# Optimization experiments

Measured on AMD Instinct MI355X. Metric: run time of the kernel, lower is better.

Reference implementation:

```python
import jax, jax.numpy as jnp
import numpy as np

B, S, D = 4, 2048, 1024
H = 16
DH = D // H


def setup_inputs() -> dict:
    key = jax.random.key(0)
    ks = jax.random.split(key, 9)
    s = 0.02
    return {
        "x": jax.random.normal(ks[0], (B, S, D), dtype=jnp.float32),
        "Wq": jax.random.normal(ks[1], (D, D), dtype=jnp.float32) * s,
        "bq": jax.random.normal(ks[2], (D,), dtype=jnp.float32) * s,
        "Wk": jax.random.normal(ks[3], (D, D), dtype=jnp.float32) * s,
        "bk": jax.random.normal(ks[4], (D,), dtype=jnp.float32) * s,
        "Wv": jax.random.normal(ks[5], (D, D), dtype=jnp.float32) * s,
        "bv": jax.random.normal(ks[6], (D,), dtype=jnp.float32) * s,
        "Wo": jax.random.normal(ks[7], (D, D), dtype=jnp.float32) * s,
        "bo": jax.random.normal(ks[8], (D,), dtype=jnp.float32) * s,
    }


def _split_heads(t):
    # [B,S,D] -> [B,H,S,DH]
    b, s, d = t.shape
    return t.reshape(b, s, H, DH).transpose(0, 2, 1, 3)


def reference(x, Wq, bq, Wk, bk, Wv, bv, Wo, bo):
    q = _split_heads(x @ Wq.T + bq)
    k = _split_heads(x @ Wk.T + bk)
    v = _split_heads(x @ Wv.T + bv)
    scale = 1.0 / np.sqrt(DH).astype(np.float32)
    scores = jnp.einsum("bhqd,bhkd->bhqk", q, k) * scale  # [B,H,S,S]
    s = scores.shape[-2]
    causal = jnp.tril(jnp.ones((s, s), dtype=bool))
    scores = jnp.where(causal[None, None], scores, -jnp.inf)
    probs = jax.nn.softmax(scores, axis=-1)
    out = jnp.einsum("bhqk,bhkd->bhqd", probs, v)  # [B,H,S,DH]
    out = out.transpose(0, 2, 1, 3).reshape(x.shape[0], s, D)
    return out @ Wo.T + bo
```

## Files before the change

### kernel.cpp

```cpp
#include <hip/hip_runtime.h>
#include <hip/hip_bf16.h>
#include <cstdint>
#include <cstddef>


typedef unsigned short u16;
typedef __bf16 bf16x8 __attribute__((ext_vector_type(8)));
typedef float  f32x4  __attribute__((ext_vector_type(4)));

__device__ __forceinline__ u16 f2bf(float f) {
  unsigned u = __float_as_uint(f);
  unsigned r = u + 0x7fffu + ((u >> 16) & 1u);
  return (u16)(r >> 16);
}

__device__ __forceinline__ void llds16(const u16* g, u16* l) {
  __builtin_amdgcn_global_load_lds(
      (const __attribute__((address_space(1))) void*)g,
      (__attribute__((address_space(3))) void*)l, 16, 0, 0);
}

__global__ void cast_bf16_kernel(const float* __restrict__ in, u16* __restrict__ out, int n4) {
  int i = blockIdx.x * blockDim.x + threadIdx.x;
  if (i >= n4) return;
  float4 f = ((const float4*)in)[i];
  ushort4 u;
  u.x = f2bf(f.x); u.y = f2bf(f.y); u.z = f2bf(f.z); u.w = f2bf(f.w);
  ((ushort4*)out)[i] = u;
}

__global__ void cast4_kernel(const float* __restrict__ a, const float* __restrict__ b,
                             const float* __restrict__ c, const float* __restrict__ d,
                             u16* __restrict__ oa, u16* __restrict__ ob,
                             u16* __restrict__ oc, u16* __restrict__ od, int n4) {
  const int w = blockIdx.y;
  const float* src = (w == 0) ? a : (w == 1) ? b : (w == 2) ? c : d;
  u16* dst = (w == 0) ? oa : (w == 1) ? ob : (w == 2) ? oc : od;
  int i = blockIdx.x * blockDim.x + threadIdx.x;
  if (i >= n4) return;
  float4 f = ((const float4*)src)[i];
  ushort4 u;
  u.x = f2bf(f.x); u.y = f2bf(f.y); u.z = f2bf(f.z); u.w = f2bf(f.w);
  ((ushort4*)dst)[i] = u;
}

__global__ __launch_bounds__(512) void gemm_qkv_256(
    const u16* __restrict__ A, const u16* __restrict__ Bw,
    const float* __restrict__ b0, const float* __restrict__ b1, const float* __restrict__ b2,
    u16* __restrict__ qkv_out)
{
  __shared__ u16 lds[57344];

  const int tid = threadIdx.x;
  const int lane = tid & 63;
  const int wave = tid >> 6;

  const int bid = (int)blockIdx.x;
  const int xcd = bid & 7;
  const int idx = bid >> 3;
  const int mt = (xcd << 2) | (idx & 3);
  const int nt = idx >> 2;
  const int m0 = mt << 8;
  const int n0 = nt * 192;

  const int warp_m = wave >> 2;
  const int warp_n = wave & 3;
  const int wm = warp_m << 7;
  const int wn = warp_n * 48;
  const int fr = lane & 15;
  const int g  = lane >> 4;

  const int srow = tid >> 3;
  const int schk = ((tid & 7) ^ (srow & 7)) << 3;
  const u16* pA = A  + (size_t)(m0 + srow) * 1024 + schk;
  const u16* pB = Bw + (size_t)(n0 + srow) * 1024 + schk;

  const int rsw0 = ((g    ) ^ (fr & 7)) << 3;
  const int rsw1 = ((g ^ 4) ^ (fr & 7)) << 3;

  const u16* Ab0 = lds + (size_t)(wm + fr) * 64;
  const u16* Bb0 = lds + 16384 + (size_t)(wn + fr) * 64;
  const u16* Ab1 = Ab0 + 28672;
  const u16* Bb1 = Bb0 + 28672;

  f32x4 acc[8][3];
  const f32x4 zero = {0.f, 0.f, 0.f, 0.f};
#pragma unroll
  for (int i = 0; i < 8; i++)
#pragma unroll
    for (int j = 0; j < 3; j++) acc[i][j] = zero;

  bf16x8 a_[4][2];
  bf16x8 b_[3][2];

  auto stageA = [&](int kt, int buf, int half) {
    const u16* src = pA + (size_t)half * 131072 + (kt << 6);
    u16* dst = lds + buf * 28672 + half * 8192 + tid * 8;
    llds16(src, dst);
    llds16(src + 65536, dst + 4096);
  };
  auto stageB0 = [&](int kt, int buf) {
    const u16* src = pB + (kt << 6);
    u16* dst = lds + buf * 28672 + 16384 + tid * 8;
    llds16(src, dst);
    llds16(src + 65536, dst + 4096);
  };
  auto stageB1 = [&](int kt, int buf) {
    const u16* src = pB + 131072 + (kt << 6);
    u16* dst = lds + buf * 28672 + 24576 + tid * 8;
    llds16(src, dst);
  };
  auto loadA4 = [&](const u16* Ab, int ib) {
#pragma unroll
    for (int ii = 0; ii < 4; ii++) {
      const u16* r = Ab + (ib + ii) * 1024;
      a_[ii][0] = *(const bf16x8*)(r + rsw0);
      a_[ii][1] = *(const bf16x8*)(r + rsw1);
    }
  };
  auto loadB = [&](const u16* Bb, int j0, int nj) {
#pragma unroll
    for (int jj = 0; jj < 3; jj++) {
      if (jj < nj) {
        const u16* r = Bb + (j0 + jj) * 1024;
        b_[j0 + jj][0] = *(const bf16x8*)(r + rsw0);
        b_[j0 + jj][1] = *(const bf16x8*)(r + rsw1);
      }
    }
  };
  auto mfmaQ = [&](int ib, int j0, int nj) {
    __builtin_amdgcn_s_setprio(1);
#pragma unroll
    for (int jj = 0; jj < 3; jj++) {
      if (jj < nj) {
#pragma unroll
        for (int ii = 0; ii < 4; ii++) {
          acc[ib+ii][j0+jj] = __builtin_amdgcn_mfma_f32_16x16x32_bf16(
              a_[ii][0], b_[j0+jj][0], acc[ib+ii][j0+jj], 0, 0, 0);
          acc[ib+ii][j0+jj] = __builtin_amdgcn_mfma_f32_16x16x32_bf16(
              a_[ii][1], b_[j0+jj][1], acc[ib+ii][j0+jj], 0, 0, 0);
        }
      }
    }
    __builtin_amdgcn_s_setprio(0);
  };

  stageA(0, 0, 0);
  stageA(0, 0, 1);
  stageB0(0, 0);
  stageB1(0, 0);
  stageA(1, 1, 0);
  asm volatile("s_waitcnt vmcnt(2)" ::: "memory");
  __builtin_amdgcn_s_barrier();

  const int NTI = 8;
  for (int t = 0; t < NTI; ++t) {
    const bool st = (t < NTI - 1);
    const int ka = 2 * t + 1;
    const int kb = 2 * t + 2;
    const int kc = 2 * t + 3;

    loadA4(Ab0, 0); loadB(Bb0, 0, 2);
    stageA(ka, 1, 1);
    __builtin_amdgcn_s_barrier();
    mfmaQ(0, 0, 2);
    __builtin_amdgcn_s_barrier();
    loadB(Bb0, 2, 1);
    stageB0(ka, 1);
    __builtin_amdgcn_s_barrier();
    mfmaQ(0, 2, 1);
    __builtin_amdgcn_s_barrier();
    loadA4(Ab0, 4);
    stageB1(ka, 1);
    __builtin_amdgcn_s_barrier();
    mfmaQ(4, 2, 1);
    __builtin_amdgcn_s_barrier();
    if (st) stageA(kb, 0, 0);
    __builtin_amdgcn_s_barrier();
    mfmaQ(4, 0, 2);
    if (st) { asm volatile("s_waitcnt vmcnt(2)" ::: "memory"); }
    else    { asm volatile("s_waitcnt vmcnt(0)" ::: "memory"); }
    __builtin_amdgcn_s_barrier();

    loadA4(Ab1, 0); loadB(Bb1, 0, 2);
    if (st) stageA(kb, 0, 1);
    __builtin_amdgcn_s_barrier();
    mfmaQ(0, 0, 2);
    __builtin_amdgcn_s_barrier();
    loadB(Bb1, 2, 1);
    if (st) stageB0(kb, 0);
    __builtin_amdgcn_s_barrier();
    mfmaQ(0, 2, 1);
    __builtin_amdgcn_s_barrier();
    loadA4(Ab1, 4);
    if (st) stageB1(kb, 0);
    __builtin_amdgcn_s_barrier();
    mfmaQ(4, 2, 1);
    __builtin_amdgcn_s_barrier();
    if (st) stageA(kc, 1, 0);
    __builtin_amdgcn_s_barrier();
    mfmaQ(4, 0, 2);
    if (st) { asm volatile("s_waitcnt vmcnt(2)" ::: "memory"); }
    __builtin_amdgcn_s_barrier();
  }

  __syncthreads();
  const int bI  = m0 >> 11;
  const int s0m = m0 & 2047;
#pragma unroll
  for (int j = 0; j < 3; j++) {
    const int ncol = n0 + wn + j * 16 + fr;
    const int which = ncol >> 10;
    const float bb = ((which == 0) ? b0 : (which == 1) ? b1 : b2)[ncol & 1023];
    const float post = (which == 0) ? 0.18033688011f : 1.0f;
    const int cl = wn + j * 16 + fr;
#pragma unroll
    for (int i = 0; i < 8; i++) {
#pragma unroll
      for (int r = 0; r < 4; r++) {
        const int row = wm + i * 16 + g * 4 + r;
        lds[row * 200 + cl] = f2bf((acc[i][j][r] + bb) * post);
      }
    }
  }
  __syncthreads();
  const int part = tid & 7;
#pragma unroll
  for (int p = 0; p < 12; p++) {
    const int hc = p >> 2;
    const int ml = ((p & 3) << 6) + (tid >> 3);
    const int ncol0 = n0 + hc * 64;
    const int which = ncol0 >> 10;
    const int h = (ncol0 >> 6) & 15;
    const bf16x8 v = *(const bf16x8*)(lds + ml * 200 + hc * 64 + part * 8);
    *(bf16x8*)(qkv_out + (size_t)which * 8388608 +
               ((size_t)(bI * 16 + h) * 2048 + s0m + ml) * 64 + part * 8) = v;
  }
}

__global__ __launch_bounds__(256) void gemm_bt(
    const u16* __restrict__ A, const u16* __restrict__ Bw,
    const float* __restrict__ b0, const float* __restrict__ b1, const float* __restrict__ b2,
    u16* __restrict__ qkv_out, float* __restrict__ flat_out,
    int K, int mode)
{
  __shared__ u16 As[128 * 32];
  __shared__ u16 Bs[128 * 32];

  const int tid = threadIdx.x;
  const int n0 = blockIdx.x * 128;
  const int m0 = blockIdx.y * 128;

  const int srow = tid >> 2;
  const int soff = (tid & 3) * 8;
  const u16* gA0 = A  + (size_t)(m0 + srow) * K + soff;
  const u16* gA1 = gA0 + (size_t)64 * K;
  const u16* gB0 = Bw + (size_t)(n0 + srow) * K + soff;
  const u16* gB1 = gB0 + (size_t)64 * K;
  u16* lA0 = As + tid * 8;
  u16* lA1 = As + 2048 + tid * 8;
  u16* lB0 = Bs + tid * 8;
  u16* lB1 = Bs + 2048 + tid * 8;

  const int lane = tid & 63;
  const int wave = tid >> 6;
  const int wm = (wave >> 1) * 64;
  const int wn = (wave & 1) * 64;
  const int fr = lane & 15;
  const int k8 = (lane >> 4) * 8;

  f32x4 zero = {0.f, 0.f, 0.f, 0.f};
  f32x4 acc[4][4];
#pragma unroll
  for (int i = 0; i < 4; i++)
#pragma unroll
    for (int j = 0; j < 4; j++) acc[i][j] = zero;

  for (int k0 = 0; k0 < K; k0 += 32) {
    llds16(gA0 + k0, lA0);
    llds16(gA1 + k0, lA1);
    llds16(gB0 + k0, lB0);
    llds16(gB1 + k0, lB1);
    __syncthreads();
    bf16x8 af[4], bfr[4];
#pragma unroll
    for (int i = 0; i < 4; i++)
      af[i] = *(const bf16x8*)(As + (wm + i * 16 + fr) * 32 + k8);
#pragma unroll
    for (int j = 0; j < 4; j++)
      bfr[j] = *(const bf16x8*)(Bs + (wn + j * 16 + fr) * 32 + k8);
#pragma unroll
    for (int i = 0; i < 4; i++)
#pragma unroll
      for (int j = 0; j < 4; j++)
        acc[i][j] = __builtin_amdgcn_mfma_f32_16x16x32_bf16(af[i], bfr[j], acc[i][j], 0, 0, 0);
    __syncthreads();
  }

  const int rbase = (lane >> 4) * 4;
  if (mode == 0) {
    const int which = n0 >> 10;
    const float* bias = (which == 0) ? b0 : ((which == 1) ? b1 : b2);
    const float post = (which == 0) ? 0.18033688011f : 1.0f;
    u16* outb = qkv_out + (size_t)which * 8388608;
#pragma unroll
    for (int j = 0; j < 4; j++) {
      const int nn = (n0 + wn + j * 16 + fr) & 1023;
      const float bb = bias[nn];
      const int h = nn >> 6, dh = nn & 63;
#pragma unroll
      for (int i = 0; i < 4; i++) {
#pragma unroll
        for (int r = 0; r < 4; r++) {
          const int m = m0 + wm + i * 16 + rbase + r;
          const int bI = m >> 11, s = m & 2047;
          outb[(((size_t)bI * 16 + h) * 2048 + s) * 64 + dh] = f2bf((acc[i][j][r] + bb) * post);
        }
      }
    }
  } else {
#pragma unroll
    for (int j = 0; j < 4; j++) {
      const int n = n0 + wn + j * 16 + fr;
      const float bb = b0[n];
#pragma unroll
      for (int i = 0; i < 4; i++) {
#pragma unroll
        for (int r = 0; r < 4; r++) {
          const int m = m0 + wm + i * 16 + rbase + r;
          flat_out[(size_t)m * 1024 + n] = acc[i][j][r] + bb;
        }
      }
    }
  }
}

__global__ __launch_bounds__(256) void transpose_v(const u16* __restrict__ V, u16* __restrict__ VT) {
  __shared__ u16 t_s[64 * 72];
  const int tid = threadIdx.x;
  const int st = blockIdx.x << 6;
  const int bh = blockIdx.y;
  const u16* src = V + ((size_t)bh * 2048 + st) * 64;
#pragma unroll
  for (int p = 0; p < 2; p++) {
    int i = p * 256 + tid;
    int row = i >> 3, ch = i & 7;
    bf16x8 v = *(const bf16x8*)(src + row * 64 + ch * 8);
    *(bf16x8*)(t_s + row * 72 + ch * 8) = v;
  }
  __syncthreads();
  u16* dst = VT + (size_t)bh * 131072 + st;
#pragma unroll
  for (int p = 0; p < 2; p++) {
    int i = p * 256 + tid;
    int dh = i >> 3, ch = i & 7;
    union { u16 s[8]; bf16x8 v; } u;
#pragma unroll
    for (int e = 0; e < 8; e++) u.s[e] = t_s[(ch * 8 + e) * 72 + dh];
    *(bf16x8*)(dst + (size_t)dh * 2048 + ch * 8) = u.v;
  }
}

__global__ __launch_bounds__(256, 3) void attn_fa(
    const u16* __restrict__ Qb, const u16* __restrict__ Kb,
    const u16* __restrict__ VT, u16* __restrict__ Ob)
{
  __shared__ u16 k_s[2 * 4096];
  __shared__ u16 v_s[2 * 4096];
  __shared__ u16 p_s[128 * 72];
  __shared__ float l_s[128];

  const int tid = threadIdx.x;
  const int lane = tid & 63;
  const int wave = tid >> 6;
  const int bid = (int)blockIdx.x;
  const int qt = 15 - (bid >> 6);
  const int bh = (((bid >> 3) & 7) << 3) | (bid & 7);
  const size_t head = (size_t)bh << 17;
  const int fr = lane & 15;
  const int g = lane >> 4;
  const int k8 = g << 3;
  const int q0 = qt << 7;
  const int wrow = wave << 5;

  bf16x8 aq[2][2];
#pragma unroll
  for (int f = 0; f < 2; f++) {
    const u16* qp = Qb + head + (size_t)(q0 + wrow + (f << 4) + fr) * 64;
    aq[f][0] = *(const bf16x8*)(qp + k8);
    aq[f][1] = *(const bf16x8*)(qp + 32 + k8);
  }

  const int r0 = tid >> 3, c0 = tid & 7;
  const int r1 = 32 + r0;
  const int koff0 = r0 * 64 + (((c0 ^ r0) & 7) << 3);
  const int koff1 = r1 * 64 + (((c0 ^ r1) & 7) << 3);
  const int voff0 = r0 * 2048 + (((c0 ^ r0) & 7) << 3);
  const int voff1 = r1 * 2048 + (((c0 ^ r1) & 7) << 3);
  int kaddr[4][2], vaddr[2][4];
#pragma unroll
  for (int j = 0; j < 4; j++) {
    const int kn = (j << 4) + fr;
    kaddr[j][0] = kn * 64 + (((g ^ kn) & 7) << 3);
    kaddr[j][1] = kn * 64 + ((((g + 4) ^ kn) & 7) << 3);
#pragma unroll
    for (int s2 = 0; s2 < 2; s2++)
      vaddr[s2][j] = kn * 64 + ((((s2 << 2) + g) ^ (kn & 7)) << 3);
  }
  u16* const prow0 = p_s + (wrow + fr) * 72;
  u16* const prow1 = p_s + (wrow + 16 + fr) * 72;
  const u16* Kbase = Kb + head;
  const u16* Vbase = VT + head;

  auto issueK = [&](int jt2, int buf) {
    const u16* Kt = Kbase + ((size_t)jt2 << 12);
    llds16(Kt + koff0, k_s + (buf << 12) + tid * 8);
    llds16(Kt + koff1, k_s + (buf << 12) + 2048 + tid * 8);
  };
  auto issueV = [&](int jt2, int buf) {
    const u16* Vt = Vbase + (jt2 << 6);
    llds16(Vt + voff0, v_s + (buf << 12) + tid * 8);
    llds16(Vt + voff1, v_s + (buf << 12) + 2048 + tid * 8);
  };

  f32x4 o_acc[2][4];
  const f32x4 zero = {0.f, 0.f, 0.f, 0.f};
#pragma unroll
  for (int f = 0; f < 2; f++)
#pragma unroll
    for (int j = 0; j < 4; j++) o_acc[f][j] = zero;
  float l_run[2] = {0.f, 0.f};

  const int jmax = 2 * qt + 1;
  const int jt_diag = 2 * qt + (wave >> 1);

  auto do_pv = [&](const u16* vs) {
#pragma unroll
    for (int s2 = 0; s2 < 2; s2++) {
      const bf16x8 ap0 = *(const bf16x8*)(prow0 + (s2 << 5) + k8);
      const bf16x8 ap1 = *(const bf16x8*)(prow1 + (s2 << 5) + k8);
#pragma unroll
      for (int j = 0; j < 4; j++) {
        const bf16x8 bv = *(const bf16x8*)(vs + vaddr[s2][j]);
        o_acc[0][j] = __builtin_amdgcn_mfma_f32_16x16x32_bf16(ap0, bv, o_acc[0][j], 0, 0, 0);
        o_acc[1][j] = __builtin_amdgcn_mfma_f32_16x16x32_bf16(ap1, bv, o_acc[1][j], 0, 0, 0);
      }
    }
  };

  auto do_s = [&](const u16* ks, bool dodiag, int jt) {
    f32x4 s_acc[2][4];
#pragma unroll
    for (int f = 0; f < 2; f++)
#pragma unroll
      for (int j = 0; j < 4; j++) s_acc[f][j] = zero;
#pragma unroll
    for (int j = 0; j < 4; j++) {
      const bf16x8 ka0 = *(const bf16x8*)(ks + kaddr[j][0]);
      const bf16x8 ka1 = *(const bf16x8*)(ks + kaddr[j][1]);
      s_acc[0][j] = __builtin_amdgcn_mfma_f32_16x16x32_bf16(ka0, aq[0][0], s_acc[0][j], 0, 0, 0);
      s_acc[0][j] = __builtin_amdgcn_mfma_f32_16x16x32_bf16(ka1, aq[0][1], s_acc[0][j], 0, 0, 0);
      s_acc[1][j] = __builtin_amdgcn_mfma_f32_16x16x32_bf16(ka0, aq[1][0], s_acc[1][j], 0, 0, 0);
      s_acc[1][j] = __builtin_amdgcn_mfma_f32_16x16x32_bf16(ka1, aq[1][1], s_acc[1][j], 0, 0, 0);
    }
#pragma unroll
    for (int f = 0; f < 2; f++) {
      const int qa = q0 + wrow + (f << 4) + fr;
      u16* prow = (f == 0) ? prow0 : prow1;
      if (dodiag) {
#pragma unroll
        for (int j = 0; j < 4; j++) {
          const int kb = (jt << 6) + (j << 4) + (g << 2);
          float p0 = (kb + 0 > qa) ? 0.f : __builtin_amdgcn_exp2f(s_acc[f][j][0]);
          float p1 = (kb + 1 > qa) ? 0.f : __builtin_amdgcn_exp2f(s_acc[f][j][1]);
          float p2 = (kb + 2 > qa) ? 0.f : __builtin_amdgcn_exp2f(s_acc[f][j][2]);
          float p3 = (kb + 3 > qa) ? 0.f : __builtin_amdgcn_exp2f(s_acc[f][j][3]);
          l_run[f] += (p0 + p1) + (p2 + p3);
          union { __hip_bfloat162 h; unsigned u; } ca, cb;
          ca.h = __float22bfloat162_rn(make_float2(p0, p1));
          cb.h = __float22bfloat162_rn(make_float2(p2, p3));
          *(uint2*)(prow + (j << 4) + (g << 2)) = make_uint2(ca.u, cb.u);
        }
      } else {
#pragma unroll
        for (int j = 0; j < 4; j++) {
          float p0 = __builtin_amdgcn_exp2f(s_acc[f][j][0]);
          float p1 = __builtin_amdgcn_exp2f(s_acc[f][j][1]);
          float p2 = __builtin_amdgcn_exp2f(s_acc[f][j][2]);
          float p3 = __builtin_amdgcn_exp2f(s_acc[f][j][3]);
          l_run[f] += (p0 + p1) + (p2 + p3);
          union { __hip_bfloat162 h; unsigned u; } ca, cb;
          ca.h = __float22bfloat162_rn(make_float2(p0, p1));
          cb.h = __float22bfloat162_rn(make_float2(p2, p3));
          *(uint2*)(prow + (j << 4) + (g << 2)) = make_uint2(ca.u, cb.u);
        }
      }
    }
  };

  issueK(0, 0);

  for (int jt = 0; jt <= jmax; jt++) {
    const int kb = jt & 1;
    __syncthreads();
    if (jt < jmax) issueK(jt + 1, kb ^ 1);
    issueV(jt, kb);
    if (jt > 0 && jt - 1 <= jt_diag) do_pv(v_s + ((kb ^ 1) << 12));
    if (jt <= jt_diag) do_s(k_s + (kb << 12), jt == jt_diag, jt);
  }
  __syncthreads();
  if (jt_diag == jmax) do_pv(v_s + ((jmax & 1) << 12));

#pragma unroll
  for (int f = 0; f < 2; f++) {
    float l = l_run[f];
    l += __shfl_xor(l, 16);
    l += __shfl_xor(l, 32);
    if (g == 0) l_s[wrow + (f << 4) + fr] = l;
  }
  const int b = bh >> 4, h = bh & 15;
#pragma unroll
  for (int f = 0; f < 2; f++) {
#pragma unroll
    for (int r = 0; r < 4; r++) {
      const int qloc = wrow + (f << 4) + (g << 2) + r;
      const float inv = 1.f / l_s[qloc];
      const int q_abs = q0 + qloc;
#pragma unroll
      for (int j = 0; j < 4; j++)
        Ob[((size_t)b * 2048 + q_abs) * 1024 + (h << 6) + (j << 4) + fr] =
            f2bf(o_acc[f][j][r] * inv);
    }
  }
}

extern "C" void kernel_launch(void* const* d_in, const int* in_sizes, int n_in,
                              void* d_out, int out_size, void* d_ws, size_t ws_size,
                              hipStream_t stream) {
  const float* x  = (const float*)d_in[0];
  const float* Wq = (const float*)d_in[1];
  const float* bq = (const float*)d_in[2];
  const float* Wk = (const float*)d_in[3];
  const float* bk = (const float*)d_in[4];
  const float* Wv = (const float*)d_in[5];
  const float* bv = (const float*)d_in[6];
  const float* Wo = (const float*)d_in[7];
  const float* bo = (const float*)d_in[8];
  float* out = (float*)d_out;

  char* ws = (char*)d_ws;
  u16* xb    = (u16*)(ws);
  u16* vT    = (u16*)(ws);
  u16* wqkv  = (u16*)(ws + 16777216);
  u16* wo    = (u16*)(ws + 23068672);
  u16* qkv   = (u16*)(ws + 25165824);
  u16* attnb = (u16*)(ws + 75497472);

  cast_bf16_kernel<<<8192, 256, 0, stream>>>(x, xb, 2097152);
  cast4_kernel<<<dim3(1024, 4), 256, 0, stream>>>(
      Wq, Wk, Wv, Wo, wqkv, wqkv + 1048576, wqkv + 2097152, wo, 262144);

  gemm_qkv_256<<<dim3(512), 512, 0, stream>>>(xb, wqkv, bq, bk, bv, qkv);

  transpose_v<<<dim3(32, 64), 256, 0, stream>>>(qkv + 16777216, vT);

  attn_fa<<<dim3(1024), 256, 0, stream>>>(qkv, qkv + 8388608, vT, attnb);

  gemm_bt<<<dim3(8, 64), 256, 0, stream>>>(attnb, wo, bo, bo, bo, nullptr, out, 1024, 1);
}
```

Before: 247.7 us.

## Replace output projection GEMM with pipelined 256x128 tile kernel and reorder QKV MFMA phases

The simple 128x128 output-projection GEMM, which loaded one K=32 slice per step with full syncs, is replaced by a 512-thread 256x128-tile kernel. The new kernel uses swizzled LDS double buffering, direct global-to-LDS loads interleaved with MFMA phases, and an XCD-aware block mapping. The QKV GEMM's MFMA schedule is also reordered so all 8 A fragments stay in registers and the third B column is done in one pass. This costs more registers in exchange for fewer LDS reloads. The aim is to raise MFMA utilisation and cut synchronisation and memory stalls in both GEMMs.

After: 242.0 us. 1.02x faster.

```diff
diff --git a/kernel.cpp b/kernel.cpp
--- a/kernel.cpp
+++ b/kernel.cpp
@@ -90,7 +90,7 @@
 #pragma unroll
     for (int j = 0; j < 3; j++) acc[i][j] = zero;
 
-  bf16x8 a_[4][2];
+  bf16x8 a_[8][2];
   bf16x8 b_[3][2];
 
   auto stageA = [&](int kt, int buf, int half) {
@@ -114,8 +114,8 @@
 #pragma unroll
     for (int ii = 0; ii < 4; ii++) {
       const u16* r = Ab + (ib + ii) * 1024;
-      a_[ii][0] = *(const bf16x8*)(r + rsw0);
-      a_[ii][1] = *(const bf16x8*)(r + rsw1);
+      a_[ib + ii][0] = *(const bf16x8*)(r + rsw0);
+      a_[ib + ii][1] = *(const bf16x8*)(r + rsw1);
     }
   };
   auto loadB = [&](const u16* Bb, int j0, int nj) {
@@ -128,19 +128,27 @@
       }
     }
   };
-  auto mfmaQ = [&](int ib, int j0, int nj) {
+  auto mfmaJ01 = [&](int ib) {
     __builtin_amdgcn_s_setprio(1);
 #pragma unroll
-    for (int jj = 0; jj < 3; jj++) {
-      if (jj < nj) {
-#pragma unroll
-        for (int ii = 0; ii < 4; ii++) {
-          acc[ib+ii][j0+jj] = __builtin_amdgcn_mfma_f32_16x16x32_bf16(
-              a_[ii][0], b_[j0+jj][0], acc[ib+ii][j0+jj], 0, 0, 0);
-          acc[ib+ii][j0+jj] = __builtin_amdgcn_mfma_f32_16x16x32_bf16(
-              a_[ii][1], b_[j0+jj][1], acc[ib+ii][j0+jj], 0, 0, 0);
-        }
+    for (int jj = 0; jj < 2; jj++)
+#pragma unroll
+      for (int ii = 0; ii < 4; ii++) {
+        acc[ib+ii][jj] = __builtin_amdgcn_mfma_f32_16x16x32_bf16(
+            a_[ib+ii][0], b_[jj][0], acc[ib+ii][jj], 0, 0, 0);
+        acc[ib+ii][jj] = __builtin_amdgcn_mfma_f32_16x16x32_bf16(
+            a_[ib+ii][1], b_[jj][1], acc[ib+ii][jj], 0, 0, 0);
       }
+    __builtin_amdgcn_s_setprio(0);
+  };
+  auto mfmaJ2 = [&]() {
+    __builtin_amdgcn_s_setprio(1);
+#pragma unroll
+    for (int ii = 0; ii < 8; ii++) {
+      acc[ii][2] = __builtin_amdgcn_mfma_f32_16x16x32_bf16(
+          a_[ii][0], b_[2][0], acc[ii][2], 0, 0, 0);
+      acc[ii][2] = __builtin_amdgcn_mfma_f32_16x16x32_bf16(
+          a_[ii][1], b_[2][1], acc[ii][2], 0, 0, 0);
     }
     __builtin_amdgcn_s_setprio(0);
   };
@@ -163,21 +171,18 @@
     loadA4(Ab0, 0); loadB(Bb0, 0, 2);
     stageA(ka, 1, 1);
     __builtin_amdgcn_s_barrier();
-    mfmaQ(0, 0, 2);
+    mfmaJ01(0);
+    __builtin_amdgcn_s_barrier();
+    loadA4(Ab0, 4);
+    stageB0(ka, 1);
+    __builtin_amdgcn_s_barrier();
+    mfmaJ01(4);
     __builtin_amdgcn_s_barrier();
     loadB(Bb0, 2, 1);
-    stageB0(ka, 1);
-    __builtin_amdgcn_s_barrier();
-    mfmaQ(0, 2, 1);
-    __builtin_amdgcn_s_barrier();
-    loadA4(Ab0, 4);
     stageB1(ka, 1);
-    __builtin_amdgcn_s_barrier();
-    mfmaQ(4, 2, 1);
-    __builtin_amdgcn_s_barrier();
     if (st) stageA(kb, 0, 0);
     __builtin_amdgcn_s_barrier();
-    mfmaQ(4, 0, 2);
+    mfmaJ2();
     if (st) { asm volatile("s_waitcnt vmcnt(2)" ::: "memory"); }
     else    { asm volatile("s_waitcnt vmcnt(0)" ::: "memory"); }
     __builtin_amdgcn_s_barrier();
@@ -185,21 +190,17 @@
     loadA4(Ab1, 0); loadB(Bb1, 0, 2);
     if (st) stageA(kb, 0, 1);
     __builtin_amdgcn_s_barrier();
-    mfmaQ(0, 0, 2);
+    mfmaJ01(0);
+    __builtin_amdgcn_s_barrier();
+    loadA4(Ab1, 4);
+    if (st) stageB0(kb, 0);
+    __builtin_amdgcn_s_barrier();
+    mfmaJ01(4);
     __builtin_amdgcn_s_barrier();
     loadB(Bb1, 2, 1);
-    if (st) stageB0(kb, 0);
-    __builtin_amdgcn_s_barrier();
-    mfmaQ(0, 2, 1);
-    __builtin_amdgcn_s_barrier();
-    loadA4(Ab1, 4);
-    if (st) stageB1(kb, 0);
-    __builtin_amdgcn_s_barrier();
-    mfmaQ(4, 2, 1);
-    __builtin_amdgcn_s_barrier();
-    if (st) stageA(kc, 1, 0);
-    __builtin_amdgcn_s_barrier();
-    mfmaQ(4, 0, 2);
+    if (st) { stageB1(kb, 0); stageA(kc, 1, 0); }
+    __builtin_amdgcn_s_barrier();
+    mfmaJ2();
     if (st) { asm volatile("s_waitcnt vmcnt(2)" ::: "memory"); }
     __builtin_amdgcn_s_barrier();
   }
@@ -238,98 +239,165 @@
   }
 }
 
-__global__ __launch_bounds__(256) void gemm_bt(
+__global__ __launch_bounds__(512) void gemm_o_256(
     const u16* __restrict__ A, const u16* __restrict__ Bw,
-    const float* __restrict__ b0, const float* __restrict__ b1, const float* __restrict__ b2,
-    u16* __restrict__ qkv_out, float* __restrict__ flat_out,
-    int K, int mode)
+    const float* __restrict__ bo, float* __restrict__ out)
 {
-  __shared__ u16 As[128 * 32];
-  __shared__ u16 Bs[128 * 32];
+  __shared__ u16 lds[49152];
 
   const int tid = threadIdx.x;
-  const int n0 = blockIdx.x * 128;
-  const int m0 = blockIdx.y * 128;
-
-  const int srow = tid >> 2;
-  const int soff = (tid & 3) * 8;
-  const u16* gA0 = A  + (size_t)(m0 + srow) * K + soff;
-  const u16* gA1 = gA0 + (size_t)64 * K;
-  const u16* gB0 = Bw + (size_t)(n0 + srow) * K + soff;
-  const u16* gB1 = gB0 + (size_t)64 * K;
-  u16* lA0 = As + tid * 8;
-  u16* lA1 = As + 2048 + tid * 8;
-  u16* lB0 = Bs + tid * 8;
-  u16* lB1 = Bs + 2048 + tid * 8;
-
   const int lane = tid & 63;
   const int wave = tid >> 6;
-  const int wm = (wave >> 1) * 64;
-  const int wn = (wave & 1) * 64;
+
+  const int bid = (int)blockIdx.x;
+  const int xcd = bid & 7;
+  const int idx = bid >> 3;
+  const int mt = (xcd << 2) | (idx & 3);
+  const int nt = idx >> 2;
+  const int m0 = mt << 8;
+  const int n0 = nt << 7;
+
+  const int warp_m = wave >> 2;
+  const int warp_n = wave & 3;
+  const int wm = warp_m << 7;
+  const int wn = warp_n << 5;
   const int fr = lane & 15;
-  const int k8 = (lane >> 4) * 8;
-
-  f32x4 zero = {0.f, 0.f, 0.f, 0.f};
-  f32x4 acc[4][4];
-#pragma unroll
-  for (int i = 0; i < 4; i++)
-#pragma unroll
-    for (int j = 0; j < 4; j++) acc[i][j] = zero;
-
-  for (int k0 = 0; k0 < K; k0 += 32) {
-    llds16(gA0 + k0, lA0);
-    llds16(gA1 + k0, lA1);
-    llds16(gB0 + k0, lB0);
-    llds16(gB1 + k0, lB1);
-    __syncthreads();
-    bf16x8 af[4], bfr[4];
-#pragma unroll
-    for (int i = 0; i < 4; i++)
-      af[i] = *(const bf16x8*)(As + (wm + i * 16 + fr) * 32 + k8);
-#pragma unroll
-    for (int j = 0; j < 4; j++)
-      bfr[j] = *(const bf16x8*)(Bs + (wn + j * 16 + fr) * 32 + k8);
-#pragma unroll
-    for (int i = 0; i < 4; i++)
-#pragma unroll
-      for (int j = 0; j < 4; j++)
-        acc[i][j] = __builtin_amdgcn_mfma_f32_16x16x32_bf16(af[i], bfr[j], acc[i][j], 0, 0, 0);
-    __syncthreads();
-  }
-
-  const int rbase = (lane >> 4) * 4;
-  if (mode == 0) {
-    const int which = n0 >> 10;
-    const float* bias = (which == 0) ? b0 : ((which == 1) ? b1 : b2);
-    const float post = (which == 0) ? 0.18033688011f : 1.0f;
-    u16* outb = qkv_out + (size_t)which * 8388608;
-#pragma unroll
-    for (int j = 0; j < 4; j++) {
-      const int nn = (n0 + wn + j * 16 + fr) & 1023;
-      const float bb = bias[nn];
-      const int h = nn >> 6, dh = nn & 63;
-#pragma unroll
-      for (int i = 0; i < 4; i++) {
-#pragma unroll
-        for (int r = 0; r < 4; r++) {
-          const int m = m0 + wm + i * 16 + rbase + r;
-          const int bI = m >> 11, s = m & 2047;
-          outb[(((size_t)bI * 16 + h) * 2048 + s) * 64 + dh] = f2bf((acc[i][j][r] + bb) * post);
-        }
+  const int g  = lane >> 4;
+
+  const int srow = tid >> 3;
+  const int schk = ((tid & 7) ^ (srow & 7)) << 3;
+  const u16* pA = A  + (size_t)(m0 + srow) * 1024 + schk;
+  const u16* pB = Bw + (size_t)(n0 + srow) * 1024 + schk;
+
+  const int rsw0 = ((g    ) ^ (fr & 7)) << 3;
+  const int rsw1 = ((g ^ 4) ^ (fr & 7)) << 3;
+
+  const u16* Ab0 = lds + (size_t)(wm + fr) * 64;
+  const u16* Bb0 = lds + 16384 + (size_t)(wn + fr) * 64;
+  const u16* Ab1 = Ab0 + 24576;
+  const u16* Bb1 = Bb0 + 24576;
+
+  f32x4 acc[8][2];
+  const f32x4 zero = {0.f, 0.f, 0.f, 0.f};
+#pragma unroll
+  for (int i = 0; i < 8; i++)
+#pragma unroll
+    for (int j = 0; j < 2; j++) acc[i][j] = zero;
+
+  bf16x8 a_[8][2];
+  bf16x8 b_[2][2];
+
+  auto stageA = [&](int kt, int buf, int half) {
+    const u16* src = pA + (size_t)half * 131072 + (kt << 6);
+    u16* dst = lds + buf * 24576 + half * 8192 + tid * 8;
+    llds16(src, dst);
+    llds16(src + 65536, dst + 4096);
+  };
+  auto stageB = [&](int kt, int buf) {
+    const u16* src = pB + (kt << 6);
+    u16* dst = lds + buf * 24576 + 16384 + tid * 8;
+    llds16(src, dst);
+    llds16(src + 65536, dst + 4096);
+  };
+  auto loadA4 = [&](const u16* Ab, int ib) {
+#pragma unroll
+    for (int ii = 0; ii < 4; ii++) {
+      const u16* r = Ab + (ib + ii) * 1024;
+      a_[ib + ii][0] = *(const bf16x8*)(r + rsw0);
+      a_[ib + ii][1] = *(const bf16x8*)(r + rsw1);
+    }
+  };
+  auto loadB2 = [&](const u16* Bb) {
+#pragma unroll
+    for (int jj = 0; jj < 2; jj++) {
+      const u16* r = Bb + jj * 1024;
+      b_[jj][0] = *(const bf16x8*)(r + rsw0);
+      b_[jj][1] = *(const bf16x8*)(r + rsw1);
+    }
+  };
+  auto mfma16 = [&](int ib) {
+    __builtin_amdgcn_s_setprio(1);
+#pragma unroll
+    for (int jj = 0; jj < 2; jj++)
+#pragma unroll
+      for (int ii = 0; ii < 4; ii++) {
+        acc[ib+ii][jj] = __builtin_amdgcn_mfma_f32_16x16x32_bf16(
+            a_[ib+ii][0], b_[jj][0], acc[ib+ii][jj], 0, 0, 0);
+        acc[ib+ii][jj] = __builtin_amdgcn_mfma_f32_16x16x32_bf16(
+            a_[ib+ii][1], b_[jj][1], acc[ib+ii][jj], 0, 0, 0);
       }
-    }
-  } else {
-#pragma unroll
-    for (int j = 0; j < 4; j++) {
-      const int n = n0 + wn + j * 16 + fr;
-      const float bb = b0[n];
-#pragma unroll
-      for (int i = 0; i < 4; i++) {
-#pragma unroll
-        for (int r = 0; r < 4; r++) {
-          const int m = m0 + wm + i * 16 + rbase + r;
-          flat_out[(size_t)m * 1024 + n] = acc[i][j][r] + bb;
-        }
+    __builtin_amdgcn_s_setprio(0);
+  };
+  auto mfma8 = [&](int ib, int jj) {
+    __builtin_amdgcn_s_setprio(1);
+#pragma unroll
+    for (int ii = 0; ii < 4; ii++) {
+      acc[ib+ii][jj] = __builtin_amdgcn_mfma_f32_16x16x32_bf16(
+          a_[ib+ii][0], b_[jj][0], acc[ib+ii][jj], 0, 0, 0);
+      acc[ib+ii][jj] = __builtin_amdgcn_mfma_f32_16x16x32_bf16(
+          a_[ib+ii][1], b_[jj][1], acc[ib+ii][jj], 0, 0, 0);
+    }
+    __builtin_amdgcn_s_setprio(0);
+  };
+
+  stageA(0, 0, 0);
+  stageA(0, 0, 1);
+  stageB(0, 0);
+  stageA(1, 1, 0);
+  asm volatile("s_waitcnt vmcnt(2)" ::: "memory");
+  __builtin_amdgcn_s_barrier();
+
+  const int NTI = 8;
+  for (int t = 0; t < NTI; ++t) {
+    const bool st = (t < NTI - 1);
+    const int ka = 2 * t + 1;
+    const int kb = 2 * t + 2;
+    const int kc = 2 * t + 3;
+
+    loadA4(Ab0, 0); loadB2(Bb0);
+    stageA(ka, 1, 1);
+    __builtin_amdgcn_s_barrier();
+    mfma16(0);
+    __builtin_amdgcn_s_barrier();
+    loadA4(Ab0, 4);
+    stageB(ka, 1);
+    __builtin_amdgcn_s_barrier();
+    mfma8(4, 0);
+    __builtin_amdgcn_s_barrier();
+    if (st) stageA(kb, 0, 0);
+    __builtin_amdgcn_s_barrier();
+    mfma8(4, 1);
+    if (st) { asm volatile("s_waitcnt vmcnt(2)" ::: "memory"); }
+    else    { asm volatile("s_waitcnt vmcnt(0)" ::: "memory"); }
+    __builtin_amdgcn_s_barrier();
+
+    loadA4(Ab1, 0); loadB2(Bb1);
+    if (st) stageA(kb, 0, 1);
+    __builtin_amdgcn_s_barrier();
+    mfma16(0);
+    __builtin_amdgcn_s_barrier();
+    loadA4(Ab1, 4);
+    if (st) stageB(kb, 0);
+    __builtin_amdgcn_s_barrier();
+    mfma8(4, 0);
+    __builtin_amdgcn_s_barrier();
+    if (st) stageA(kc, 1, 0);
+    __builtin_amdgcn_s_barrier();
+    mfma8(4, 1);
+    if (st) { asm volatile("s_waitcnt vmcnt(2)" ::: "memory"); }
+    __builtin_amdgcn_s_barrier();
+  }
+
+#pragma unroll
+  for (int j = 0; j < 2; j++) {
+    const int n = n0 + wn + j * 16 + fr;
+    const float bb = bo[n];
+#pragma unroll
+    for (int i = 0; i < 8; i++) {
+#pragma unroll
+      for (int r = 0; r < 4; r++) {
+        const int m = m0 + wm + i * 16 + g * 4 + r;
+        out[(size_t)m * 1024 + n] = acc[i][j][r] + bb;
       }
     }
   }
@@ -566,5 +634,5 @@
 
   attn_fa<<<dim3(1024), 256, 0, stream>>>(qkv, qkv + 8388608, vT, attnb);
 
-  gemm_bt<<<dim3(8, 64), 256, 0, stream>>>(attnb, wo, bo, bo, bo, nullptr, out, 1024, 1);
-}
+  gemm_o_256<<<dim3(256), 512, 0, stream>>>(attnb, wo, bo, out);
+}
```
